# Performance work log

Hardware: AMD Instinct MI355X
Metric: run time of the kernel (lower is better)

## Reference

```python
import jax, jax.numpy as jnp
import numpy as np

# Complete A-ary tree of depth D, nodes stored in level order.
# Children of node i are A*i+1 .. A*i+A.
B, A, D = 512, 4, 6
N = (A**D - 1) // (A - 1)  # 1365 nodes per tree
V, E_EMB, E_ENC = 50000, 128, 128


def setup_inputs() -> dict:
    key = jax.random.key(0)
    ks = jax.random.split(key, 5)
    tokens = jax.random.randint(ks[0], (B, N), 0, V)
    emb = jax.random.normal(ks[1], (V, E_EMB), jnp.float32) * 0.02
    Wc_W = jax.random.normal(ks[2], (E_ENC, E_EMB), jnp.float32) / np.sqrt(E_EMB)
    Wc_b = jnp.zeros((E_ENC,), jnp.float32)
    Ws_W = jax.random.normal(ks[3], (E_ENC, E_ENC), jnp.float32) / np.sqrt(E_ENC)
    Ws_b = jnp.zeros((E_ENC,), jnp.float32)
    return {"tokens": tokens, "emb": emb, "Wc_W": Wc_W, "Wc_b": Wc_b,
            "Ws_W": Ws_W, "Ws_b": Ws_b, "bs": B}


def reference(tokens, emb, Wc_W, Wc_b, Ws_W, Ws_b, bs):
    # Per-node local term: W_c(embedding(token))  -> [B, N, E]
    e = emb[tokens] @ Wc_W.T + Wc_b
    level_sizes = [A ** d for d in range(D)]
    starts = np.cumsum([0] + level_sizes)  # static offsets into level order

    # Bottom-up recurrence: h(node) = e(node) + sum_children W_sum(h(child)).
    # W_sum (incl. bias) is applied per child then summed, matching the
    # per-child-slot index_copy + Linear in the original recursion.
    hs = [None] * D
    hs[D - 1] = e[:, starts[D - 1]:starts[D]]  # leaves
    for d in range(D - 2, -1, -1):
        child = hs[d + 1]                        # [B, A^(d+1), E]
        proj = child @ Ws_W.T + Ws_b             # W_sum per child
        agg = proj.reshape(bs, level_sizes[d], A, E_ENC).sum(axis=2)
        hs[d] = e[:, starts[d]:starts[d + 1]] + agg

    h_all = jnp.concatenate(hs, axis=1)          # [B, N, E]
    # node_list holds activation(h) per tree position; combine = max over nodes
    return jnp.max(jax.nn.relu(h_all), axis=1)   # [B, E]
```

## Files before the change

### kernel.cpp

```cpp
#include <hip/hip_runtime.h>
#include <hip/hip_bf16.h>

#define NTOK 1365
#define ED   128
#define STR  136

typedef __attribute__((ext_vector_type(8))) short short8;
typedef __attribute__((ext_vector_type(4))) float f32x4;

#define MFMA(a,b,c) __builtin_amdgcn_mfma_f32_16x16x32_bf16((a),(b),(c),0,0,0)

__device__ __forceinline__ ushort f2bf(float f) {
  union { float f; unsigned u; } v; v.f = f;
  unsigned r = v.u + 0x7fffu + ((v.u >> 16) & 1u);
  return (ushort)(r >> 16);
}
__device__ __forceinline__ ushort4 cvt4(float4 f) {
  ushort4 u; u.x = f2bf(f.x); u.y = f2bf(f.y); u.z = f2bf(f.z); u.w = f2bf(f.w);
  return u;
}
__device__ __forceinline__ short8 pack8(float4 a, float4 b) {
  union { ushort us[8]; short8 s8; } t;
  t.us[0]=f2bf(a.x); t.us[1]=f2bf(a.y); t.us[2]=f2bf(a.z); t.us[3]=f2bf(a.w);
  t.us[4]=f2bf(b.x); t.us[5]=f2bf(b.y); t.us[6]=f2bf(b.z); t.us[7]=f2bf(b.w);
  return t.s8;
}

#define SM_BYTES (4096 + 404 * STR * 2)

__global__ __attribute__((amdgpu_flat_work_group_size(512, 512),
                          amdgpu_waves_per_eu(2, 8)))
void tree_kernel(
    const int* __restrict__ tokens, const float* __restrict__ emb,
    const float* __restrict__ WcW,  const float* __restrict__ Wcb,
    const float* __restrict__ WsW,  const float* __restrict__ Wsb,
    float* __restrict__ out) {
  extern __shared__ char smem[];
  float*  PM  = (float*)smem;
  ushort* WsL = (ushort*)(PM + 1024);
  ushort* Xe0 = WsL + 128*STR;
  ushort* Xe1 = Xe0 + 64*STR;
  ushort* CS4 = Xe1 + 64*STR;
  ushort* CS3 = CS4 + 64*STR;
  ushort* CS2 = CS3 + 64*STR;
  ushort* CS1 = CS2 + 16*STR;

  const int  tid = threadIdx.x;
  const int  b   = blockIdx.x;
  const long tokbase = (long)b * NTOK;
  const int  w    = tid >> 6;
  const int  lane = tid & 63;
  const int  n16  = lane & 15;
  const int  quad = lane >> 4;
  const int  mtg  = w >> 2, ntg = w & 3;
  const int  kof  = quad * 8;

  float bcv[2], bsv[2];
  #pragma unroll
  for (int j = 0; j < 2; j++) {
    const int c = ntg*32 + j*16 + n16;
    bcv[j] = Wcb[c]; bsv[j] = 4.f * Wsb[c];
  }

  short8 Bc[2][4];
  #pragma unroll
  for (int jt = 0; jt < 2; jt++)
    #pragma unroll
    for (int kb = 0; kb < 4; kb++) {
      const float* pc = WcW + (ntg*32 + jt*16 + n16)*ED + kb*32 + kof;
      Bc[jt][kb] = pack8(((const float4*)pc)[0], ((const float4*)pc)[1]);
    }

  #pragma unroll
  for (int i = 0; i < 8; i++) {
    const int idx = tid + i*512;
    float4 f = ((const float4*)WsW)[idx];
    *(ushort4*)(WsL + (idx >> 5)*STR + ((idx & 31) << 2)) = cvt4(f);
  }

  for (int i = tid; i < 1024; i += 512) PM[i] = 0.f;

  float pm[2] = {0.f, 0.f};

  float4 RA[4], RB[4];
  auto issue64 = [&](float4 (&R)[4], int ofs) {
    const int r = tid >> 3, p = tid & 7;
    const float4* src = (const float4*)(emb + (long)tokens[tokbase + ofs + r]*ED) + (p << 2);
    R[0] = src[0]; R[1] = src[1]; R[2] = src[2]; R[3] = src[3];
  };
  auto store64 = [&](const float4 (&R)[4], ushort* Xe) {
    const int r = tid >> 3, p = tid & 7;
    short8* d = (short8*)(Xe + r*STR + (p << 4));
    d[0] = pack8(R[0], R[1]); d[1] = pack8(R[2], R[3]);
  };
  auto issueN = [&](float4 (&R)[4], int ofs, int nrows) {
    const int r = tid >> 5, p = tid & 31;
    if (r < nrows) R[0] = ((const float4*)(emb + (long)tokens[tokbase + ofs + r]*ED))[p];
  };
  auto storeN = [&](const float4 (&R)[4], ushort* Xe, int nrows) {
    const int r = tid >> 5, p = tid & 31;
    if (r < nrows) *(ushort4*)(Xe + r*STR + (p << 2)) = cvt4(R[0]);
  };

  auto phase64 = [&](const ushort* Xe, const ushort* csrc, ushort* csdst, int csrow0) {
    f32x4 acc[2][2];
    #pragma unroll
    for (int i = 0; i < 2; i++)
      #pragma unroll
      for (int j = 0; j < 2; j++) acc[i][j] = (f32x4){0.f,0.f,0.f,0.f};
    #pragma unroll
    for (int kb = 0; kb < 4; kb++) {
      const int ko = kb*32 + kof;
      short8 a0 = *(const short8*)(Xe + (mtg*32      + n16)*STR + ko);
      short8 a1 = *(const short8*)(Xe + (mtg*32 + 16 + n16)*STR + ko);
      acc[0][0]=MFMA(a0,Bc[0][kb],acc[0][0]); acc[0][1]=MFMA(a0,Bc[1][kb],acc[0][1]);
      acc[1][0]=MFMA(a1,Bc[0][kb],acc[1][0]); acc[1][1]=MFMA(a1,Bc[1][kb],acc[1][1]);
      if (csrc) {
        short8 c0 = *(const short8*)(csrc + (mtg*32      + n16)*STR + ko);
        short8 c1 = *(const short8*)(csrc + (mtg*32 + 16 + n16)*STR + ko);
        short8 s0 = *(const short8*)(WsL  + (ntg*32      + n16)*STR + ko);
        short8 s1 = *(const short8*)(WsL  + (ntg*32 + 16 + n16)*STR + ko);
        acc[0][0]=MFMA(c0,s0,acc[0][0]); acc[0][1]=MFMA(c0,s1,acc[0][1]);
        acc[1][0]=MFMA(c1,s0,acc[1][0]); acc[1][1]=MFMA(c1,s1,acc[1][1]);
      }
    }
    #pragma unroll
    for (int i = 0; i < 2; i++) {
      const int p = mtg*8 + i*4 + quad;
      #pragma unroll
      for (int j = 0; j < 2; j++) {
        const float bb = csrc ? (bcv[j] + bsv[j]) : bcv[j];
        f32x4 A = acc[i][j];
        float h0=A[0]+bb, h1=A[1]+bb, h2=A[2]+bb, h3=A[3]+bb;
        pm[j] = fmaxf(pm[j], fmaxf(fmaxf(h0,h1), fmaxf(h2,h3)));
        csdst[(csrow0 + p)*STR + ntg*32 + j*16 + n16] =
            f2bf(A[0]+A[1]+A[2]+A[3] + 4.f*bb);
      }
    }
  };

  auto smallphase = [&](const ushort* Xe, const ushort* csrc, int M, ushort* csdst) {
    if (mtg != 0) return;
    const int ar = (M == 16) ? n16 : ((M == 4) ? (n16 & 3) : 0);
    f32x4 acc[2];
    acc[0] = (f32x4){0.f,0.f,0.f,0.f}; acc[1] = (f32x4){0.f,0.f,0.f,0.f};
    #pragma unroll
    for (int kb = 0; kb < 4; kb++) {
      const int ko = kb*32 + kof;
      short8 a  = *(const short8*)(Xe   + ar*STR + ko);
      short8 c2 = *(const short8*)(csrc + ar*STR + ko);
      short8 s0 = *(const short8*)(WsL + (ntg*32      + n16)*STR + ko);
      short8 s1 = *(const short8*)(WsL + (ntg*32 + 16 + n16)*STR + ko);
      acc[0] = MFMA(a,  Bc[0][kb], acc[0]); acc[1] = MFMA(a,  Bc[1][kb], acc[1]);
      acc[0] = MFMA(c2, s0, acc[0]);        acc[1] = MFMA(c2, s1, acc[1]);
    }
    #pragma unroll
    for (int j = 0; j < 2; j++) {
      const float bb = bcv[j] + bsv[j];
      f32x4 A = acc[j];
      const int c = ntg*32 + j*16 + n16;
      if (M == 16) {
        float h0=A[0]+bb, h1=A[1]+bb, h2=A[2]+bb, h3=A[3]+bb;
        pm[j] = fmaxf(pm[j], fmaxf(fmaxf(h0,h1), fmaxf(h2,h3)));
        csdst[quad*STR + c] = f2bf(A[0]+A[1]+A[2]+A[3] + 4.f*bb);
      } else if (M == 4) {
        if (quad == 0) {
          float h0=A[0]+bb, h1=A[1]+bb, h2=A[2]+bb, h3=A[3]+bb;
          pm[j] = fmaxf(pm[j], fmaxf(fmaxf(h0,h1), fmaxf(h2,h3)));
          csdst[c] = f2bf(A[0]+A[1]+A[2]+A[3] + 4.f*bb);
        }
      } else {
        if (quad == 0) pm[j] = fmaxf(pm[j], A[0] + bb);
      }
    }
  };

  issue64(RA, 341);
  issue64(RB, 341 + 64);
  store64(RA, Xe0);
  __syncthreads();
   issue64(RA, 341+128);     phase64(Xe0, nullptr, CS4,  0); store64(RB, Xe1); __syncthreads();
   issue64(RB, 341+192);     phase64(Xe1, nullptr, CS4, 16); store64(RA, Xe0); __syncthreads();
   issue64(RA, 85);          phase64(Xe0, nullptr, CS4, 32); store64(RB, Xe1); __syncthreads();
   issue64(RB, 341+256);     phase64(Xe1, nullptr, CS4, 48); store64(RA, Xe0); __syncthreads();
   issue64(RA, 341+256+64);   phase64(Xe0, CS4,     CS3,  0); store64(RB, Xe1); __syncthreads();
   issue64(RB, 341+256+128); phase64(Xe1, nullptr, CS4,  0); store64(RA, Xe0); __syncthreads();
   issue64(RA, 341+256+192); phase64(Xe0, nullptr, CS4, 16); store64(RB, Xe1); __syncthreads();
   issue64(RB, 85+64);       phase64(Xe1, nullptr, CS4, 32); store64(RA, Xe0); __syncthreads();
   issue64(RA, 341+512);     phase64(Xe0, nullptr, CS4, 48); store64(RB, Xe1); __syncthreads();
   issue64(RB, 341+512+64);   phase64(Xe1, CS4,     CS3, 16); store64(RA, Xe0); __syncthreads();
   issue64(RA, 341+512+128); phase64(Xe0, nullptr, CS4,  0); store64(RB, Xe1); __syncthreads();
   issue64(RB, 341+512+192); phase64(Xe1, nullptr, CS4, 16); store64(RA, Xe0); __syncthreads();
   issue64(RA, 85+128);      phase64(Xe0, nullptr, CS4, 32); store64(RB, Xe1); __syncthreads();
   issue64(RB, 341+768);     phase64(Xe1, nullptr, CS4, 48); store64(RA, Xe0); __syncthreads();
   issue64(RA, 341+768+64);   phase64(Xe0, CS4,     CS3, 32); store64(RB, Xe1); __syncthreads();
   issue64(RB, 341+768+128); phase64(Xe1, nullptr, CS4,  0); store64(RA, Xe0); __syncthreads();
   issue64(RA, 341+768+192); phase64(Xe0, nullptr, CS4, 16); store64(RB, Xe1); __syncthreads();
   issue64(RB, 85+192);      phase64(Xe1, nullptr, CS4, 32); store64(RA, Xe0); __syncthreads();
   issue64(RA, 21);          phase64(Xe0, nullptr, CS4, 48); store64(RB, Xe1); __syncthreads();
   issueN(RB, 5, 16);         phase64(Xe1, CS4,     CS3, 48); store64(RA, Xe0); __syncthreads();
   issueN(RA, 1, 4);          phase64(Xe0, CS3,     CS2,  0); storeN(RB, Xe1, 16); __syncthreads();
   issueN(RB, 0, 1);          smallphase(Xe1, CS2, 16, CS1);  storeN(RA, Xe0, 4);  __syncthreads();
                              smallphase(Xe0, CS1, 4,  CS2);  storeN(RB, Xe1, 1);  __syncthreads();
                              smallphase(Xe1, CS2, 1,  nullptr);

  #pragma unroll
  for (int j = 0; j < 2; j++) {
    float v = pm[j];
    v = fmaxf(v, __shfl_xor(v, 16, 64));
    v = fmaxf(v, __shfl_xor(v, 32, 64));
    if (quad == 0) PM[w*128 + ntg*32 + j*16 + n16] = v;
  }
  __syncthreads();
  if (tid < 128) {
    float m = 0.f;
    #pragma unroll
    for (int r = 0; r < 8; r++) m = fmaxf(m, PM[r*128 + tid]);
    out[(long)b*ED + tid] = m;
  }
}

extern "C" void kernel_launch(void* const* d_in, const int* in_sizes, int n_in,
                              void* d_out, int out_size, void* d_ws, size_t ws_size,
                              hipStream_t stream) {
  const int*   tokens = (const int*)d_in[0];
  const float* emb    = (const float*)d_in[1];
  const float* WcW    = (const float*)d_in[2];
  const float* Wcb    = (const float*)d_in[3];
  const float* WsW    = (const float*)d_in[4];
  const float* Wsb    = (const float*)d_in[5];
  float* out = (float*)d_out;
  (void)d_ws; (void)ws_size;

  hipFuncSetAttribute(reinterpret_cast<const void*>(tree_kernel),
                      hipFuncAttributeMaxDynamicSharedMemorySize, SM_BYTES);
  tree_kernel<<<512, 512, SM_BYTES, stream>>>(tokens, emb, WcW, Wcb, WsW, Wsb, out);
}
```

Measured before the change: 147.6 us.

## Precompute W_c projection of the vocabulary table, then gather projected bf16 rows

```diff
diff --git a/kernel.cpp b/kernel.cpp
--- a/kernel.cpp
+++ b/kernel.cpp
@@ -4,6 +4,8 @@
 #define NTOK 1365
 #define ED   128
 #define STR  136
+#define VROWS 50000
+#define PROWS 50048
 
 typedef __attribute__((ext_vector_type(8))) short short8;
 typedef __attribute__((ext_vector_type(4))) float f32x4;
@@ -24,6 +26,248 @@
   t.us[0]=f2bf(a.x); t.us[1]=f2bf(a.y); t.us[2]=f2bf(a.z); t.us[3]=f2bf(a.w);
   t.us[4]=f2bf(b.x); t.us[5]=f2bf(b.y); t.us[6]=f2bf(b.z); t.us[7]=f2bf(b.w);
   return t.s8;
+}
+
+__global__ __attribute__((amdgpu_flat_work_group_size(256, 256)))
+void proj_kernel(const float* __restrict__ emb, const float* __restrict__ WcW,
+                 const float* __restrict__ Wcb, ushort* __restrict__ P) {
+  const int tid = threadIdx.x, w = tid >> 6, lane = tid & 63;
+  const int n16 = lane & 15, quad = lane >> 4, kof = quad * 8;
+  const int m0 = blockIdx.x * 64;
+
+  float bv[2];
+  short8 Bp[2][4];
+  #pragma unroll
+  for (int j = 0; j < 2; j++) {
+    const int c = w*32 + j*16 + n16;
+    bv[j] = Wcb[c];
+    #pragma unroll
+    for (int kb = 0; kb < 4; kb++) {
+      const float* pc = WcW + c*ED + kb*32 + kof;
+      Bp[j][kb] = pack8(((const float4*)pc)[0], ((const float4*)pc)[1]);
+    }
+  }
+  #pragma unroll
+  for (int i = 0; i < 4; i++) {
+    int arow = m0 + i*16 + n16; if (arow >= VROWS) arow = 0;
+    f32x4 acc0 = (f32x4){0.f,0.f,0.f,0.f}, acc1 = (f32x4){0.f,0.f,0.f,0.f};
+    #pragma unroll
+    for (int kb = 0; kb < 4; kb++) {
+      const float* pa = emb + (long)arow*ED + kb*32 + kof;
+      short8 a = pack8(((const float4*)pa)[0], ((const float4*)pa)[1]);
+      acc0 = MFMA(a, Bp[0][kb], acc0);
+      acc1 = MFMA(a, Bp[1][kb], acc1);
+    }
+    #pragma unroll
+    for (int r = 0; r < 4; r++) {
+      const int orow = m0 + i*16 + quad*4 + r;
+      if (orow < VROWS) {
+        P[(long)orow*ED + w*32 + n16]      = f2bf(acc0[r] + bv[0]);
+        P[(long)orow*ED + w*32 + 16 + n16] = f2bf(acc1[r] + bv[1]);
+      }
+    }
+  }
+}
+
+#define SMP_BYTES (4096 + 276 * STR * 2)
+
+__global__ __attribute__((amdgpu_flat_work_group_size(512, 512),
+                          amdgpu_waves_per_eu(4, 8)))
+void tree_kernel_p(
+    const int* __restrict__ tokens, const ushort* __restrict__ P,
+    const float* __restrict__ WsW,  const float* __restrict__ Wsb,
+    float* __restrict__ out) {
+  extern __shared__ char smem[];
+  float*  PM  = (float*)smem;
+  ushort* Xe0 = (ushort*)(PM + 1024);
+  ushort* Xe1 = Xe0 + 64*STR;
+  ushort* CS4 = Xe1 + 64*STR;
+  ushort* CS3 = CS4 + 64*STR;
+  ushort* CS2 = CS3 + 64*STR;
+  ushort* CS1 = CS2 + 16*STR;
+
+  const int  tid = threadIdx.x;
+  const int  b   = blockIdx.x;
+  const long tokbase = (long)b * NTOK;
+  const int  w    = tid >> 6;
+  const int  lane = tid & 63;
+  const int  n16  = lane & 15;
+  const int  quad = lane >> 4;
+  const int  mtg  = w >> 2, ntg = w & 3;
+  const int  kof  = quad * 8;
+
+  float bsv[2];
+  #pragma unroll
+  for (int j = 0; j < 2; j++) bsv[j] = 4.f * Wsb[ntg*32 + j*16 + n16];
+
+  short8 Bs[2][4];
+  #pragma unroll
+  for (int jt = 0; jt < 2; jt++)
+    #pragma unroll
+    for (int kb = 0; kb < 4; kb++) {
+      const float* pc = WsW + (ntg*32 + jt*16 + n16)*ED + kb*32 + kof;
+      Bs[jt][kb] = pack8(((const float4*)pc)[0], ((const float4*)pc)[1]);
+    }
+
+  short8 I2[2];
+  #pragma unroll
+  for (int j = 0; j < 2; j++) {
+    union { ushort us[8]; short8 s8; } t;
+    #pragma unroll
+    for (int e = 0; e < 8; e++) t.us[e] = 0;
+    if (quad == 2*j + (n16 >> 3)) t.us[n16 & 7] = 0x3F80;
+    I2[j] = t.s8;
+  }
+
+  for (int i = tid; i < 1024; i += 512) PM[i] = 0.f;
+  float pm[2] = {0.f, 0.f};
+
+  short8 RA[2], RB[2];
+  auto issue64 = [&](short8 (&R)[2], int ofs) {
+    const int r = tid >> 3, p = tid & 7;
+    const short8* src = (const short8*)(P + (long)tokens[tokbase + ofs + r]*ED) + (p << 1);
+    R[0] = src[0]; R[1] = src[1];
+  };
+  auto store64 = [&](const short8 (&R)[2], ushort* Xe) {
+    const int r = tid >> 3, p = tid & 7;
+    short8* d = (short8*)(Xe + r*STR + (p << 4));
+    d[0] = R[0]; d[1] = R[1];
+  };
+  auto issueN = [&](short8 (&R)[2], int ofs, int nrows) {
+    const int r = tid >> 5, p = tid & 31;
+    if (r < nrows) {
+      ushort4 v = *((const ushort4*)(P + (long)tokens[tokbase + ofs + r]*ED) + p);
+      R[0][0] = (short)v.x; R[0][1] = (short)v.y;
+      R[0][2] = (short)v.z; R[0][3] = (short)v.w;
+    }
+  };
+  auto storeN = [&](const short8 (&R)[2], ushort* Xe, int nrows) {
+    const int r = tid >> 5, p = tid & 31;
+    if (r < nrows) {
+      ushort4 v; v.x = (ushort)R[0][0]; v.y = (ushort)R[0][1];
+      v.z = (ushort)R[0][2]; v.w = (ushort)R[0][3];
+      *(ushort4*)(Xe + r*STR + (p << 2)) = v;
+    }
+  };
+
+  auto phase64 = [&](const ushort* Xe, const ushort* csrc, ushort* csdst, int csrow0) {
+    f32x4 acc[2][2];
+    #pragma unroll
+    for (int i = 0; i < 2; i++)
+      #pragma unroll
+      for (int j = 0; j < 2; j++) acc[i][j] = (f32x4){0.f,0.f,0.f,0.f};
+    {
+      const int ko = ntg*32 + kof;
+      short8 a0 = *(const short8*)(Xe + (mtg*32      + n16)*STR + ko);
+      short8 a1 = *(const short8*)(Xe + (mtg*32 + 16 + n16)*STR + ko);
+      acc[0][0]=MFMA(a0,I2[0],acc[0][0]); acc[0][1]=MFMA(a0,I2[1],acc[0][1]);
+      acc[1][0]=MFMA(a1,I2[0],acc[1][0]); acc[1][1]=MFMA(a1,I2[1],acc[1][1]);
+    }
+    if (csrc) {
+      #pragma unroll
+      for (int kb = 0; kb < 4; kb++) {
+        const int ko = kb*32 + kof;
+        short8 c0 = *(const short8*)(csrc + (mtg*32      + n16)*STR + ko);
+        short8 c1 = *(const short8*)(csrc + (mtg*32 + 16 + n16)*STR + ko);
+        acc[0][0]=MFMA(c0,Bs[0][kb],acc[0][0]); acc[0][1]=MFMA(c0,Bs[1][kb],acc[0][1]);
+        acc[1][0]=MFMA(c1,Bs[0][kb],acc[1][0]); acc[1][1]=MFMA(c1,Bs[1][kb],acc[1][1]);
+      }
+    }
+    #pragma unroll
+    for (int i = 0; i < 2; i++) {
+      const int p = mtg*8 + i*4 + quad;
+      #pragma unroll
+      for (int j = 0; j < 2; j++) {
+        const float bb = csrc ? bsv[j] : 0.f;
+        f32x4 A = acc[i][j];
+        float h0=A[0]+bb, h1=A[1]+bb, h2=A[2]+bb, h3=A[3]+bb;
+        pm[j] = fmaxf(pm[j], fmaxf(fmaxf(h0,h1), fmaxf(h2,h3)));
+        csdst[(csrow0 + p)*STR + ntg*32 + j*16 + n16] =
+            f2bf(A[0]+A[1]+A[2]+A[3] + 4.f*bb);
+      }
+    }
+  };
+
+  auto smallphase = [&](const ushort* Xe, const ushort* csrc, int M, ushort* csdst) {
+    if (mtg != 0) return;
+    const int ar = (M == 16) ? n16 : ((M == 4) ? (n16 & 3) : 0);
+    f32x4 acc[2];
+    acc[0] = (f32x4){0.f,0.f,0.f,0.f}; acc[1] = (f32x4){0.f,0.f,0.f,0.f};
+    {
+      const int ko = ntg*32 + kof;
+      short8 a = *(const short8*)(Xe + ar*STR + ko);
+      acc[0] = MFMA(a, I2[0], acc[0]); acc[1] = MFMA(a, I2[1], acc[1]);
+    }
+    #pragma unroll
+    for (int kb = 0; kb < 4; kb++) {
+      const int ko = kb*32 + kof;
+      short8 c2 = *(const short8*)(csrc + ar*STR + ko);
+      acc[0] = MFMA(c2, Bs[0][kb], acc[0]); acc[1] = MFMA(c2, Bs[1][kb], acc[1]);
+    }
+    #pragma unroll
+    for (int j = 0; j < 2; j++) {
+      const float bb = bsv[j];
+      f32x4 A = acc[j];
+      const int c = ntg*32 + j*16 + n16;
+      if (M == 16) {
+        float h0=A[0]+bb, h1=A[1]+bb, h2=A[2]+bb, h3=A[3]+bb;
+        pm[j] = fmaxf(pm[j], fmaxf(fmaxf(h0,h1), fmaxf(h2,h3)));
+        csdst[quad*STR + c] = f2bf(A[0]+A[1]+A[2]+A[3] + 4.f*bb);
+      } else if (M == 4) {
+        if (quad == 0) {
+          float h0=A[0]+bb, h1=A[1]+bb, h2=A[2]+bb, h3=A[3]+bb;
+          pm[j] = fmaxf(pm[j], fmaxf(fmaxf(h0,h1), fmaxf(h2,h3)));
+          csdst[c] = f2bf(A[0]+A[1]+A[2]+A[3] + 4.f*bb);
+        }
+      } else {
+        if (quad == 0) pm[j] = fmaxf(pm[j], A[0] + bb);
+      }
+    }
+  };
+
+  issue64(RA, 341);
+  issue64(RB, 341 + 64);
+  store64(RA, Xe0);
+  __syncthreads();
+   issue64(RA, 341+128);     phase64(Xe0, nullptr, CS4,  0); store64(RB, Xe1); __syncthreads();
+   issue64(RB, 341+192);     phase64(Xe1, nullptr, CS4, 16); store64(RA, Xe0); __syncthreads();
+   issue64(RA, 85);          phase64(Xe0, nullptr, CS4, 32); store64(RB, Xe1); __syncthreads();
+   issue64(RB, 341+256);     phase64(Xe1, nullptr, CS4, 48); store64(RA, Xe0); __syncthreads();
+   issue64(RA, 341+256+64);  phase64(Xe0, CS4,     CS3,  0); store64(RB, Xe1); __syncthreads();
+   issue64(RB, 341+256+128); phase64(Xe1, nullptr, CS4,  0); store64(RA, Xe0); __syncthreads();
+   issue64(RA, 341+256+192); phase64(Xe0, nullptr, CS4, 16); store64(RB, Xe1); __syncthreads();
+   issue64(RB, 85+64);       phase64(Xe1, nullptr, CS4, 32); store64(RA, Xe0); __syncthreads();
+   issue64(RA, 341+512);     phase64(Xe0, nullptr, CS4, 48); store64(RB, Xe1); __syncthreads();
+   issue64(RB, 341+512+64);  phase64(Xe1, CS4,     CS3, 16); store64(RA, Xe0); __syncthreads();
+   issue64(RA, 341+512+128); phase64(Xe0, nullptr, CS4,  0); store64(RB, Xe1); __syncthreads();
+   issue64(RB, 341+512+192); phase64(Xe1, nullptr, CS4, 16); store64(RA, Xe0); __syncthreads();
+   issue64(RA, 85+128);      phase64(Xe0, nullptr, CS4, 32); store64(RB, Xe1); __syncthreads();
+   issue64(RB, 341+768);     phase64(Xe1, nullptr, CS4, 48); store64(RA, Xe0); __syncthreads();
+   issue64(RA, 341+768+64);  phase64(Xe0, CS4,     CS3, 32); store64(RB, Xe1); __syncthreads();
+   issue64(RB, 341+768+128); phase64(Xe1, nullptr, CS4,  0); store64(RA, Xe0); __syncthreads();
+   issue64(RA, 341+768+192); phase64(Xe0, nullptr, CS4, 16); store64(RB, Xe1); __syncthreads();
+   issue64(RB, 85+192);      phase64(Xe1, nullptr, CS4, 32); store64(RA, Xe0); __syncthreads();
+   issue64(RA, 21);          phase64(Xe0, nullptr, CS4, 48); store64(RB, Xe1); __syncthreads();
+   issueN(RB, 5, 16);        phase64(Xe1, CS4,     CS3, 48); store64(RA, Xe0); __syncthreads();
+   issueN(RA, 1, 4);         phase64(Xe0, CS3,     CS2,  0); storeN(RB, Xe1, 16); __syncthreads();
+   issueN(RB, 0, 1);         smallphase(Xe1, CS2, 16, CS1);  storeN(RA, Xe0, 4);  __syncthreads();
+                             smallphase(Xe0, CS1, 4,  CS2);  storeN(RB, Xe1, 1);  __syncthreads();
+                             smallphase(Xe1, CS2, 1,  nullptr);
+
+  #pragma unroll
+  for (int j = 0; j < 2; j++) {
+    float v = pm[j];
+    v = fmaxf(v, __shfl_xor(v, 16, 64));
+    v = fmaxf(v, __shfl_xor(v, 32, 64));
+    if (quad == 0) PM[w*128 + ntg*32 + j*16 + n16] = v;
+  }
+  __syncthreads();
+  if (tid < 128) {
+    float m = 0.f;
+    #pragma unroll
+    for (int r = 0; r < 8; r++) m = fmaxf(m, PM[r*128 + tid]);
+    out[(long)b*ED + tid] = m;
+  }
 }
 
 #define SM_BYTES (4096 + 404 * STR * 2)
@@ -79,7 +323,6 @@
   }
 
   for (int i = tid; i < 1024; i += 512) PM[i] = 0.f;
-
   float pm[2] = {0.f, 0.f};
 
   float4 RA[4], RB[4];
@@ -179,30 +422,30 @@
   issue64(RB, 341 + 64);
   store64(RA, Xe0);
   __syncthreads();
-   issue64(RA, 341+128);     phase64(Xe0, nullptr, CS4,  0); store64(RB, Xe1); __syncthreads();
-   issue64(RB, 341+192);     phase64(Xe1, nullptr, CS4, 16); store64(RA, Xe0); __syncthreads();
-   issue64(RA, 85);          phase64(Xe0, nullptr, CS4, 32); store64(RB, Xe1); __syncthreads();
-   issue64(RB, 341+256);     phase64(Xe1, nullptr, CS4, 48); store64(RA, Xe0); __syncthreads();
-   issue64(RA, 341+256+64);   phase64(Xe0, CS4,     CS3,  0); store64(RB, Xe1); __syncthreads();
-   issue64(RB, 341+256+128); phase64(Xe1, nullptr, CS4,  0); store64(RA, Xe0); __syncthreads();
-   issue64(RA, 341+256+192); phase64(Xe0, nullptr, CS4, 16); store64(RB, Xe1); __syncthreads();
-   issue64(RB, 85+64);       phase64(Xe1, nullptr, CS4, 32); store64(RA, Xe0); __syncthreads();
-   issue64(RA, 341+512);     phase64(Xe0, nullptr, CS4, 48); store64(RB, Xe1); __syncthreads();
-   issue64(RB, 341+512+64);   phase64(Xe1, CS4,     CS3, 16); store64(RA, Xe0); __syncthreads();
-   issue64(RA, 341+512+128); phase64(Xe0, nullptr, CS4,  0); store64(RB, Xe1); __syncthreads();
-   issue64(RB, 341+512+192); phase64(Xe1, nullptr, CS4, 16); store64(RA, Xe0); __syncthreads();
-   issue64(RA, 85+128);      phase64(Xe0, nullptr, CS4, 32); store64(RB, Xe1); __syncthreads();
-   issue64(RB, 341+768);     phase64(Xe1, nullptr, CS4, 48); store64(RA, Xe0); __syncthreads();
-   issue64(RA, 341+768+64);   phase64(Xe0, CS4,     CS3, 32); store64(RB, Xe1); __syncthreads();
-   issue64(RB, 341+768+128); phase64(Xe1, nullptr, CS4,  0); store64(RA, Xe0); __syncthreads();
-   issue64(RA, 341+768+192); phase64(Xe0, nullptr, CS4, 16); store64(RB, Xe1); __syncthreads();
-   issue64(RB, 85+192);      phase64(Xe1, nullptr, CS4, 32); store64(RA, Xe0); __syncthreads();
-   issue64(RA, 21);          phase64(Xe0, nullptr, CS4, 48); store64(RB, Xe1); __syncthreads();
-   issueN(RB, 5, 16);         phase64(Xe1, CS4,     CS3, 48); store64(RA, Xe0); __syncthreads();
-   issueN(RA, 1, 4);          phase64(Xe0, CS3,     CS2,  0); storeN(RB, Xe1, 16); __syncthreads();
-   issueN(RB, 0, 1);          smallphase(Xe1, CS2, 16, CS1);  storeN(RA, Xe0, 4);  __syncthreads();
-                              smallphase(Xe0, CS1, 4,  CS2);  storeN(RB, Xe1, 1);  __syncthreads();
-                              smallphase(Xe1, CS2, 1,  nullptr);
+  issue64(RA, 341+128);     phase64(Xe0, nullptr, CS4,  0); store64(RB, Xe1); __syncthreads();
+  issue64(RB, 341+192);     phase64(Xe1, nullptr, CS4, 16); store64(RA, Xe0); __syncthreads();
+  issue64(RA, 85);          phase64(Xe0, nullptr, CS4, 32); store64(RB, Xe1); __syncthreads();
+  issue64(RB, 341+256);     phase64(Xe1, nullptr, CS4, 48); store64(RA, Xe0); __syncthreads();
+  issue64(RA, 341+256+64);  phase64(Xe0, CS4,     CS3,  0); store64(RB, Xe1); __syncthreads();
+  issue64(RB, 341+256+128); phase64(Xe1, nullptr, CS4,  0); store64(RA, Xe0); __syncthreads();
+  issue64(RA, 341+256+192); phase64(Xe0, nullptr, CS4, 16); store64(RB, Xe1); __syncthreads();
+  issue64(RB, 85+64);       phase64(Xe1, nullptr, CS4, 32); store64(RA, Xe0); __syncthreads();
+  issue64(RA, 341+512);     phase64(Xe0, nullptr, CS4, 48); store64(RB, Xe1); __syncthreads();
+  issue64(RB, 341+512+64);  phase64(Xe1, CS4,     CS3, 16); store64(RA, Xe0); __syncthreads();
+  issue64(RA, 341+512+128); phase64(Xe0, nullptr, CS4,  0); store64(RB, Xe1); __syncthreads();
+  issue64(RB, 341+512+192); phase64(Xe1, nullptr, CS4, 16); store64(RA, Xe0); __syncthreads();
+  issue64(RA, 85+128);      phase64(Xe0, nullptr, CS4, 32); store64(RB, Xe1); __syncthreads();
+  issue64(RB, 341+768);     phase64(Xe1, nullptr, CS4, 48); store64(RA, Xe0); __syncthreads();
+  issue64(RA, 341+768+64);  phase64(Xe0, CS4,     CS3, 32); store64(RB, Xe1); __syncthreads();
+  issue64(RB, 341+768+128); phase64(Xe1, nullptr, CS4,  0); store64(RA, Xe0); __syncthreads();
+  issue64(RA, 341+768+192); phase64(Xe0, nullptr, CS4, 16); store64(RB, Xe1); __syncthreads();
+  issue64(RB, 85+192);      phase64(Xe1, nullptr, CS4, 32); store64(RA, Xe0); __syncthreads();
+  issue64(RA, 21);          phase64(Xe0, nullptr, CS4, 48); store64(RB, Xe1); __syncthreads();
+  issueN(RB, 5, 16);        phase64(Xe1, CS4,     CS3, 48); store64(RA, Xe0); __syncthreads();
+  issueN(RA, 1, 4);         phase64(Xe0, CS3,     CS2,  0); storeN(RB, Xe1, 16); __syncthreads();
+  issueN(RB, 0, 1);         smallphase(Xe1, CS2, 16, CS1);  storeN(RA, Xe0, 4);  __syncthreads();
+                            smallphase(Xe0, CS1, 4,  CS2);  storeN(RB, Xe1, 1);  __syncthreads();
+                            smallphase(Xe1, CS2, 1,  nullptr);
 
   #pragma unroll
   for (int j = 0; j < 2; j++) {
@@ -230,9 +473,17 @@
   const float* WsW    = (const float*)d_in[4];
   const float* Wsb    = (const float*)d_in[5];
   float* out = (float*)d_out;
-  (void)d_ws; (void)ws_size;
-
-  hipFuncSetAttribute(reinterpret_cast<const void*>(tree_kernel),
-                      hipFuncAttributeMaxDynamicSharedMemorySize, SM_BYTES);
-  tree_kernel<<<512, 512, SM_BYTES, stream>>>(tokens, emb, WcW, Wcb, WsW, Wsb, out);
-}
+
+  const size_t needP = (size_t)PROWS * ED * sizeof(ushort);
+  if (d_ws != nullptr && ws_size >= needP) {
+    ushort* P = (ushort*)d_ws;
+    proj_kernel<<<(VROWS + 63) / 64, 256, 0, stream>>>(emb, WcW, Wcb, P);
+    hipFuncSetAttribute(reinterpret_cast<const void*>(tree_kernel_p),
+                        hipFuncAttributeMaxDynamicSharedMemorySize, SMP_BYTES);
+    tree_kernel_p<<<512, 512, SMP_BYTES, stream>>>(tokens, P, WsW, Wsb, out);
+  } else {
+    hipFuncSetAttribute(reinterpret_cast<const void*>(tree_kernel),
+                        hipFuncAttributeMaxDynamicSharedMemorySize, SM_BYTES);
+    tree_kernel<<<512, 512, SM_BYTES, stream>>>(tokens, emb, WcW, Wcb, WsW, Wsb, out);
+  }
+}
```

New measurement: 135.3 us. -8.4%, faster.
